# Performance work log

Measured on AMD Instinct MI355X. Metric: run time of the kernel, lower is better.

## Reference

```python
import jax, jax.numpy as jnp
import numpy as np

B, T, NS, NP, F, FO, K1, K2 = 128, 24, 20, 8, 256, 256, 3, 2
ES_EXTRA, EP_EXTRA = 60, 16


def _edges(n, n_extra, seed):
    # ring in both directions guarantees every node has in- and out-degree >= 1
    rng = np.random.default_rng(seed)
    i = np.arange(n)
    src = np.concatenate([i, (i + 1) % n, rng.integers(0, n, n_extra)])
    dst = np.concatenate([(i + 1) % n, i, rng.integers(0, n, n_extra)])
    return jnp.asarray(np.stack([src, dst]).astype(np.int32))


def _dconv(X, row, col, ew, W, b):
    # X: [B, N, Cin], W: [2, K, Cin, Cout]  (torch_geometric_temporal DConv)
    N = X.shape[1]
    deg_out = jnp.zeros((N,), X.dtype).at[row].add(ew)
    deg_in = jnp.zeros((N,), X.dtype).at[col].add(ew)
    norm_out = (1.0 / deg_out)[row]
    norm_in = (1.0 / deg_in)[row]

    def prop(x, norm):
        msg = x[:, row, :] * norm[None, :, None]  # gather at source, scale
        return jnp.zeros_like(x).at[:, col, :].add(msg)  # scatter-add at target

    H = X @ W[0, 0] + X @ W[1, 0]
    K = W.shape[1]
    Tx_0 = X
    if K > 1:
        Tx_1_o = prop(X, norm_out)
        Tx_1_i = prop(X, norm_in)
        H = H + Tx_1_o @ W[0, 1] + Tx_1_i @ W[1, 1]
        for k in range(2, K):
            Tx_2_o = 2.0 * prop(Tx_1_o, norm_out) - Tx_0
            Tx_2_i = 2.0 * prop(Tx_1_i, norm_in) - Tx_0
            H = H + Tx_2_o @ W[0, k] + Tx_2_i @ W[1, k]
            Tx_0, Tx_1_o, Tx_1_i = Tx_1_o, Tx_2_o, Tx_2_i
    return H + b


def _forward(x_dis, x_precip, edge_index_s, edge_weight_s, edge_index_p, edge_weight_p,
             Wz_s, bz_s, Wz_p, bz_p, Wr_s, br_s, Wr_p, br_p, Wh_s, bh_s, Wh_p, bh_p,
             W_ro, b_ro, W_ag, b_ag):
    b_, t_, ns, _ = x_dis.shape
    np_ = x_precip.shape[2]
    fo = Wz_s.shape[-1]
    rs, cs = edge_index_s[0], edge_index_s[1]
    rp, cp = edge_index_p[0], edge_index_p[1]

    def gate(Xs, Xp, Hs, Hp, Ws, bs, Wp, bp):
        Gs = _dconv(jnp.concatenate([Xs, Hs], axis=-1), rs, cs, edge_weight_s, Ws, bs)
        Gp = _dconv(jnp.concatenate([Xp, Hp], axis=-1), rp, cp, edge_weight_p, Wp, bp)
        return jnp.concatenate([Gs, Gp], axis=1)

    def step(H, xt):
        Xs, Xp = xt
        Hs, Hp = H[:, :ns], H[:, ns:]
        Z = jax.nn.sigmoid(gate(Xs, Xp, Hs, Hp, Wz_s, bz_s, Wz_p, bz_p))
        R = jax.nn.sigmoid(gate(Xs, Xp, Hs, Hp, Wr_s, br_s, Wr_p, br_p))
        gH = H * R
        Ht = jnp.tanh(gate(Xs, Xp, gH[:, :ns], gH[:, ns:], Wh_s, bh_s, Wh_p, bh_p))
        return Z * H + (1.0 - Z) * Ht, None

    H0 = jnp.zeros((b_, ns + np_, fo), x_dis.dtype)
    H, _ = jax.lax.scan(step, H0, (jnp.swapaxes(x_dis, 0, 1), jnp.swapaxes(x_precip, 0, 1)))
    out = H @ W_ro + b_ro                       # [B, 28, 1] readout per node
    out = (out[:, :, 0] @ W_ag + b_ag)[:, :, None]  # aggr over 28 nodes -> [B, 5, 1]
    return out


def setup_inputs() -> dict:
    key = jax.random.key(0)
    ks = jax.random.split(key, 24)
    sc = 0.04  # ~1/sqrt(fan_in=512)
    d = {
        'x_dis': jax.random.normal(ks[0], (B, T, NS, F), jnp.float32),
        'x_precip': jax.random.normal(ks[1], (B, T, NP, F), jnp.float32),
        'edge_index_s': _edges(NS, ES_EXTRA, 1),
        'edge_index_p': _edges(NP, EP_EXTRA, 2),
        'edge_weight_s': jax.random.uniform(ks[2], (2 * NS + ES_EXTRA,), jnp.float32, 0.1, 1.0),
        'edge_weight_p': jax.random.uniform(ks[3], (2 * NP + EP_EXTRA,), jnp.float32, 0.1, 1.0),
    }
    names_s = ['Wz_s', 'Wr_s', 'Wh_s']
    names_p = ['Wz_p', 'Wr_p', 'Wh_p']
    for i, n in enumerate(names_s):
        d[n] = sc * jax.random.normal(ks[4 + i], (2, K1, F + FO, FO), jnp.float32)
        d['b' + n[1:]] = sc * jax.random.normal(ks[7 + i], (FO,), jnp.float32)
    for i, n in enumerate(names_p):
        d[n] = sc * jax.random.normal(ks[10 + i], (2, K2, F + FO, FO), jnp.float32)
        d['b' + n[1:]] = sc * jax.random.normal(ks[13 + i], (FO,), jnp.float32)
    d['W_ro'] = sc * jax.random.normal(ks[16], (FO, 1), jnp.float32)
    d['b_ro'] = sc * jax.random.normal(ks[17], (1,), jnp.float32)
    d['W_ag'] = 0.1 * jax.random.normal(ks[18], (NS + NP, 5), jnp.float32)
    d['b_ag'] = 0.1 * jax.random.normal(ks[19], (5,), jnp.float32)
    return d


def reference(x_dis, x_precip, edge_index_s, edge_weight_s, edge_index_p, edge_weight_p,
              Wz_s, bz_s, Wz_p, bz_p, Wr_s, br_s, Wr_p, br_p, Wh_s, bh_s, Wh_p, bh_p,
              W_ro, b_ro, W_ag, b_ag):
    return _forward(x_dis, x_precip, edge_index_s, edge_weight_s, edge_index_p, edge_weight_p,
                    Wz_s, bz_s, Wz_p, bz_p, Wr_s, br_s, Wr_p, br_p, Wh_s, bh_s, Wh_p, bh_p,
                    W_ro, b_ro, W_ag, b_ag)
```

## Files before the change

### kernel.cpp

```cpp
#include <hip/hip_runtime.h>
#include <stdint.h>

#define NSN 20
#define NPN 8
#define NB 128
#define TT 24
#define NN 28
#define ES 100
#define EP 32
#define KHS 1280
#define KHP 768
#define NPRE 768
#define TCH 4

typedef _Float16 half_t;
typedef __attribute__((ext_vector_type(8))) _Float16 f16x8;
typedef __attribute__((ext_vector_type(4))) float f32x4;

__device__ __forceinline__ void gl16(const half_t* g, half_t* l) {
  __builtin_amdgcn_global_load_lds((const __attribute__((address_space(1))) void*)g,
                                   (__attribute__((address_space(3))) void*)l, 16, 0, 0);
}

__global__ void graph_build(const int* __restrict__ ei_s, const float* __restrict__ ew_s,
                            const int* __restrict__ ei_p, const float* __restrict__ ew_p,
                            float* __restrict__ Ms_s, float* __restrict__ Ms_p,
                            float* __restrict__ Mbig_s, float* __restrict__ Mbig_p) {
  __shared__ float Ao[NSN*NSN], Aiw[NSN*NSN], dgo[NSN], dgi[NSN];
  __shared__ float T2o[NSN*NSN], T2i[NSN*NSN];
  __shared__ float Aop[NPN*NPN], Aip[NPN*NPN], dgop[NPN], dgip[NPN];
  int tid = threadIdx.x;
  for (int i = tid; i < NSN*NSN; i += blockDim.x) { Ao[i] = 0.f; Aiw[i] = 0.f; }
  for (int i = tid; i < NPN*NPN; i += blockDim.x) { Aop[i] = 0.f; Aip[i] = 0.f; }
  if (tid < NSN) { dgo[tid] = 0.f; dgi[tid] = 0.f; }
  if (tid < NPN) { dgop[tid] = 0.f; dgip[tid] = 0.f; }
  __syncthreads();
  if (tid == 0) {
    for (int e = 0; e < ES; ++e) { int r = ei_s[e], c = ei_s[ES+e]; float w = ew_s[e]; dgo[r] += w; dgi[c] += w; }
    for (int e = 0; e < ES; ++e) { int r = ei_s[e], c = ei_s[ES+e]; Ao[c*NSN+r] += 1.f/dgo[r]; Aiw[c*NSN+r] += 1.f/dgi[r]; }
  }
  if (tid == 1) {
    for (int e = 0; e < EP; ++e) { int r = ei_p[e], c = ei_p[EP+e]; float w = ew_p[e]; dgop[r] += w; dgip[c] += w; }
    for (int e = 0; e < EP; ++e) { int r = ei_p[e], c = ei_p[EP+e]; Aop[c*NPN+r] += 1.f/dgop[r]; Aip[c*NPN+r] += 1.f/dgip[r]; }
  }
  __syncthreads();
  for (int i = tid; i < NSN*NSN; i += blockDim.x) {
    int r = i / NSN, c = i % NSN;
    float so = 0.f, si = 0.f;
    for (int k = 0; k < NSN; ++k) { so += Ao[r*NSN+k]*Ao[k*NSN+c]; si += Aiw[r*NSN+k]*Aiw[k*NSN+c]; }
    float t2o = 2.f*so - (r==c ? 1.f : 0.f);
    float t2i = 2.f*si - (r==c ? 1.f : 0.f);
    T2o[i] = t2o; T2i[i] = t2i;
    Ms_s[0*NSN*NSN + i] = Ao[i];
    Ms_s[1*NSN*NSN + i] = Aiw[i];
    Ms_s[2*NSN*NSN + i] = t2o;
    Ms_s[3*NSN*NSN + i] = t2i;
  }
  for (int i = tid; i < NPN*NPN; i += blockDim.x) {
    Ms_p[0*NPN*NPN + i] = Aop[i];
    Ms_p[1*NPN*NPN + i] = Aip[i];
  }
  __syncthreads();
  for (int i = tid; i < NSN*NSN*5; i += blockDim.x) {
    int n = i / 100, s = i % 100, r = s / 5, tau = s % 5;
    float v;
    if (tau == 0) v = (n == r) ? 1.f : 0.f;
    else if (tau == 1) v = Ao[n*NSN + r];
    else if (tau == 2) v = Aiw[n*NSN + r];
    else if (tau == 3) v = T2o[n*NSN + r];
    else               v = T2i[n*NSN + r];
    Mbig_s[i] = v;
  }
  for (int i = tid; i < NPN*NPN*3; i += blockDim.x) {
    int n = i / 24, s = i % 24, r = s / 3, tau = s % 3;
    float v;
    if (tau == 0) v = (n == r) ? 1.f : 0.f;
    else if (tau == 1) v = Aop[n*NPN + r];
    else               v = Aip[n*NPN + r];
    Mbig_p[i] = v;
  }
}

__device__ __forceinline__ float wsrc(const float* W, int Kdim, int tau, int i, int jj) {
  if (tau == 0) return W[(size_t)(0*Kdim+0)*512*256 + (size_t)i*256 + jj]
                     + W[(size_t)(1*Kdim+0)*512*256 + (size_t)i*256 + jj];
  int dir = (tau - 1) & 1;
  int k = (tau + 1) >> 1;
  return W[(size_t)(dir*Kdim + k)*512*256 + (size_t)i*256 + jj];
}

__global__ void prep_w(const float* __restrict__ Wz_s, const float* __restrict__ Wr_s, const float* __restrict__ Wh_s,
                       const float* __restrict__ Wz_p, const float* __restrict__ Wr_p, const float* __restrict__ Wh_p,
                       half_t* __restrict__ WX_s, half_t* __restrict__ WX_p,
                       half_t* __restrict__ WHzr_s, half_t* __restrict__ WHh_s,
                       half_t* __restrict__ WHzr_p, half_t* __restrict__ WHh_p) {
  const long c0 = (long)768*KHS;
  const long c1 = c0 + (long)768*KHP;
  const long c2 = c1 + (long)2560*256;
  const long c3 = c2 + (long)1280*256;
  const long c4 = c3 + (long)1536*256;
  const long c5 = c4 + (long)768*256;
  for (long idx = (long)blockIdx.x*256 + threadIdx.x; idx < c5; idx += (long)gridDim.x*256) {
    if (idx < c0) {
      long x = idx; int j = (int)(x / KHS), c = (int)(x % KHS); int tau = c >> 8;
      const float* W = (j < 256) ? Wz_s : (j < 512) ? Wr_s : Wh_s;
      WX_s[x] = (half_t)wsrc(W, 3, tau, c & 255, j & 255);
    } else if (idx < c1) {
      long x = idx - c0; int j = (int)(x / KHP), c = (int)(x % KHP); int tau = c >> 8;
      const float* W = (j < 256) ? Wz_p : (j < 512) ? Wr_p : Wh_p;
      WX_p[x] = (half_t)wsrc(W, 2, tau, c & 255, j & 255);
    } else if (idx < c2) {
      long x = idx - c1; int cc = (int)(x >> 8), f = (int)(x & 255);
      int tau = cc / 512, j = cc % 512;
      const float* W = (j < 256) ? Wz_s : Wr_s;
      WHzr_s[(size_t)cc*256 + f] = (half_t)wsrc(W, 3, tau, 256 + f, j & 255);
    } else if (idx < c3) {
      long x = idx - c2; int cc = (int)(x >> 8), f = (int)(x & 255);
      int tau = cc >> 8, j = cc & 255;
      WHh_s[(size_t)cc*256 + f] = (half_t)wsrc(Wh_s, 3, tau, 256 + f, j);
    } else if (idx < c4) {
      long x = idx - c3; int cc = (int)(x >> 8), f = (int)(x & 255);
      int tau = cc / 512, j = cc % 512;
      const float* W = (j < 256) ? Wz_p : Wr_p;
      WHzr_p[(size_t)cc*256 + f] = (half_t)wsrc(W, 2, tau, 256 + f, j & 255);
    } else {
      long x = idx - c4; int cc = (int)(x >> 8), f = (int)(x & 255);
      int tau = cc >> 8, j = cc & 255;
      WHh_p[(size_t)cc*256 + f] = (half_t)wsrc(Wh_p, 2, tau, 256 + f, j);
    }
  }
}

__global__ void zero_f(float* p, long n) {
  long i = (long)blockIdx.x*256 + threadIdx.x;
  if (i < n) p[i] = 0.f;
}

__global__ __launch_bounds__(256) void chebx(const float* __restrict__ xdis, const float* __restrict__ xpre,
                                             const float* __restrict__ Ms_s, const float* __restrict__ Ms_p,
                                             half_t* __restrict__ XTs, half_t* __restrict__ XTp, int t0) {
  __shared__ float Xc[NSN*256];
  __shared__ float Ml[4*NSN*NSN];
  int bb = blockIdx.x, tid = threadIdx.x;
  bool isP = bb >= NB*TCH;
  int q = isP ? bb - NB*TCH : bb;
  int b = q % NB, tp = q / NB;
  int N = isP ? NPN : NSN, nt = isP ? 3 : 5, KX = nt << 8;
  const float* X = isP ? (xpre + (size_t)(b*TT + t0 + tp)*NPN*256)
                       : (xdis + (size_t)(b*TT + t0 + tp)*NSN*256);
  for (int i = tid; i < N*64; i += 256) ((float4*)Xc)[i] = ((const float4*)X)[i];
  int nm = (nt-1)*N*N;
  const float* Msrc = isP ? Ms_p : Ms_s;
  for (int i = tid; i < nm; i += 256) Ml[i] = Msrc[i];
  __syncthreads();
  half_t* XT = isP ? XTp : XTs;
  size_t rowbase = (size_t)(tp*NB + b)*N;
  int kc8 = KX >> 3, nch = N * kc8;
  for (int i = tid; i < nch; i += 256) {
    int n = i / kc8, c8 = i - n*kc8;
    int tau = c8 >> 5, f0 = (c8 & 31) << 3;
    float v[8];
    if (tau == 0) {
      const float* xr0 = Xc + n*256 + f0;
#pragma unroll
      for (int j = 0; j < 8; ++j) v[j] = xr0[j];
    } else {
      const float* M = Ml + (tau-1)*N*N + n*N;
#pragma unroll
      for (int j = 0; j < 8; ++j) v[j] = 0.f;
      for (int r = 0; r < N; ++r) {
        float m = M[r];
        const float* xr = Xc + r*256 + f0;
#pragma unroll
        for (int j = 0; j < 8; ++j) v[j] += m*xr[j];
      }
    }
    union { uint4 q; half_t u[8]; } hv;
#pragma unroll
    for (int j = 0; j < 8; ++j) hv.u[j] = (half_t)v[j];
    *(uint4*)(XT + (rowbase + n)*(size_t)KX + ((size_t)c8 << 3)) = hv.q;
  }
}

__global__ __launch_bounds__(512) void gemm_pre(
    const half_t* __restrict__ A0, const half_t* __restrict__ B0, int K0,
    int rbS, int cbTot,
    const half_t* __restrict__ A1, const half_t* __restrict__ B1, int K1,
    half_t* __restrict__ Px0, half_t* __restrict__ Px1,
    const float* __restrict__ bz0, const float* __restrict__ br0, const float* __restrict__ bh0,
    const float* __restrict__ bz1, const float* __restrict__ br1, const float* __restrict__ bh1) {
  __shared__ __align__(16) half_t sbuf[3][12288];
  int id = blockIdx.x;
  int xx = id & 7, kq = id >> 3;
  int rbTot8 = (gridDim.x / cbTot) >> 3;
  int rb = xx*rbTot8 + kq / cbTot;
  int cb = kq - (kq / cbTot)*cbTot;

  bool isP = rb >= rbS;
  const half_t* A = isP ? A1 : A0;
  const half_t* B = isP ? B1 : B0;
  int K = isP ? K1 : K0;
  int row0 = (isP ? rb - rbS : rb) * 64;
  int col0 = cb * 128;
  int tid = threadIdx.x, lane = tid & 63, w = tid >> 6;
  int l15 = lane & 15, l4 = lane >> 4;
  int wr = (w >> 2) * 32, wc = (w & 3) * 32;

  const half_t* srcb[3];
  int ldso[3];
#pragma unroll
  for (int j = 0; j < 3; ++j) {
    int c = ((j*8 + w) << 6) + lane;
    const half_t* base;
    if (c < 512) {
      int r = c >> 3, kb = c & 7;
      base = A + (size_t)(row0 + r)*K + ((kb ^ (r & 7)) << 3);
    } else {
      int d = c - 512, r = d >> 3, kb = d & 7;
      base = B + (size_t)(col0 + r)*K + ((kb ^ (r & 7)) << 3);
    }
    srcb[j] = base;
    ldso[j] = c << 3;
  }

  f32x4 acc[2][2];
#pragma unroll
  for (int i = 0; i < 2; ++i)
#pragma unroll
    for (int j = 0; j < 2; ++j) acc[i][j] = (f32x4){0.f,0.f,0.f,0.f};

  int nk = K >> 6;
#define STAGEP(K0E, BUFP)  { half_t* _b = (BUFP); _Pragma("unroll") \
    for (int j = 0; j < 3; ++j) gl16(srcb[j] + (K0E), _b + ldso[j]); }

  STAGEP(0,   &sbuf[0][0]);
  STAGEP(64,  &sbuf[1][0]);
  STAGEP(128, &sbuf[2][0]);

  for (int k = 0; k < nk; ++k) {
    int rem = nk - 1 - k;
    if (rem >= 2)      asm volatile("s_waitcnt vmcnt(6)" ::: "memory");
    else if (rem == 1) asm volatile("s_waitcnt vmcnt(3)" ::: "memory");
    else               asm volatile("s_waitcnt vmcnt(0)" ::: "memory");
    __builtin_amdgcn_s_barrier();
    const half_t* cur = &sbuf[k % 3][0];
    const half_t* cB = cur + 4096;
#pragma unroll
    for (int kk = 0; kk < 2; ++kk) {
      f16x8 af[2], bq[2];
#pragma unroll
      for (int mi = 0; mi < 2; ++mi) {
        int r = wr + mi*16 + l15;
        int sb = (kk*4 + l4) ^ (r & 7);
        af[mi] = *(const f16x8*)&cur[r*64 + sb*8];
      }
#pragma unroll
      for (int ni = 0; ni < 2; ++ni) {
        int r = wc + ni*16 + l15;
        int sb = (kk*4 + l4) ^ (r & 7);
        bq[ni] = *(const f16x8*)&cB[r*64 + sb*8];
      }
#pragma unroll
      for (int mi = 0; mi < 2; ++mi)
#pragma unroll
        for (int ni = 0; ni < 2; ++ni)
          acc[mi][ni] = __builtin_amdgcn_mfma_f32_16x16x32_f16(af[mi], bq[ni], acc[mi][ni], 0, 0, 0);
    }
    __builtin_amdgcn_s_barrier();
    if (k + 3 < nk) STAGEP((k + 3) << 6, &sbuf[k % 3][0]);
  }
#undef STAGEP

  half_t* PxO = isP ? Px1 : Px0;
#pragma unroll
  for (int mi = 0; mi < 2; ++mi)
#pragma unroll
    for (int ni = 0; ni < 2; ++ni) {
      int colg = col0 + wc + ni*16 + l15;
      const float* bias = (colg < 256) ? (isP ? bz1 : bz0)
                        : (colg < 512) ? (isP ? br1 : br0)
                                       : (isP ? bh1 : bh0);
#pragma unroll
      for (int rg = 0; rg < 4; ++rg) {
        int grow = row0 + wr + mi*16 + l4*4 + rg;
        PxO[(size_t)grow*NPRE + colg] = (half_t)(acc[mi][ni][rg] + bias[colg & 255]);
      }
    }
}

__global__ __launch_bounds__(512) void gemm_y(
    const half_t* __restrict__ A0, const half_t* __restrict__ B0, half_t* __restrict__ C0, int NC0, int cb0, int nb0,
    const half_t* __restrict__ A1, const half_t* __restrict__ B1, half_t* __restrict__ C1, int NC1, int cb1) {
  __shared__ __align__(16) half_t sbuf[3][12288];
  int id = blockIdx.x;
  int rb, cb; const half_t *A, *B; half_t* C; int NC;
  if (id < nb0) { rb = id / cb0; cb = id % cb0; A = A0; B = B0; C = C0; NC = NC0; }
  else { int q = id - nb0; rb = q / cb1; cb = q % cb1; A = A1; B = B1; C = C1; NC = NC1; }
  int row0 = rb*64, col0 = cb*128;
  int tid = threadIdx.x, lane = tid & 63, w = tid >> 6;
  int l15 = lane & 15, l4 = lane >> 4;
  int wr = (w >> 2) * 32, wc = (w & 3) * 32;

  const half_t* srcb[3];
  int ldso[3];
#pragma unroll
  for (int j = 0; j < 3; ++j) {
    int c = ((j*8 + w) << 6) + lane;
    const half_t* base;
    if (c < 512) {
      int r = c >> 3, kb = c & 7;
      base = A + (size_t)(row0 + r)*256 + ((kb ^ (r & 7)) << 3);
    } else {
      int d = c - 512, r = d >> 3, kb = d & 7;
      base = B + (size_t)(col0 + r)*256 + ((kb ^ (r & 7)) << 3);
    }
    srcb[j] = base;
    ldso[j] = c << 3;
  }

  f32x4 acc[2][2];
#pragma unroll
  for (int i = 0; i < 2; ++i)
#pragma unroll
    for (int j = 0; j < 2; ++j) acc[i][j] = (f32x4){0.f,0.f,0.f,0.f};

#define STAGEY(K0E, BUFP)  { half_t* _b = (BUFP); _Pragma("unroll") \
    for (int j = 0; j < 3; ++j) gl16(srcb[j] + (K0E), _b + ldso[j]); }

  STAGEY(0,   &sbuf[0][0]);
  STAGEY(64,  &sbuf[1][0]);
  STAGEY(128, &sbuf[2][0]);

  for (int k = 0; k < 4; ++k) {
    int rem = 3 - k;
    if (rem >= 2)      asm volatile("s_waitcnt vmcnt(6)" ::: "memory");
    else if (rem == 1) asm volatile("s_waitcnt vmcnt(3)" ::: "memory");
    else               asm volatile("s_waitcnt vmcnt(0)" ::: "memory");
    __builtin_amdgcn_s_barrier();
    const half_t* cur = &sbuf[k % 3][0];
    const half_t* cB = cur + 4096;
#pragma unroll
    for (int kk = 0; kk < 2; ++kk) {
      f16x8 af[2], bq[2];
#pragma unroll
      for (int mi = 0; mi < 2; ++mi) {
        int r = wr + mi*16 + l15;
        int sb = (kk*4 + l4) ^ (r & 7);
        af[mi] = *(const f16x8*)&cur[r*64 + sb*8];
      }
#pragma unroll
      for (int ni = 0; ni < 2; ++ni) {
        int r = wc + ni*16 + l15;
        int sb = (kk*4 + l4) ^ (r & 7);
        bq[ni] = *(const f16x8*)&cB[r*64 + sb*8];
      }
#pragma unroll
      for (int mi = 0; mi < 2; ++mi)
#pragma unroll
        for (int ni = 0; ni < 2; ++ni)
          acc[mi][ni] = __builtin_amdgcn_mfma_f32_16x16x32_f16(af[mi], bq[ni], acc[mi][ni], 0, 0, 0);
    }
    __builtin_amdgcn_s_barrier();
    if (k + 3 < 4) STAGEY((k + 3) << 6, &sbuf[k % 3][0]);
  }
#undef STAGEY

#pragma unroll
  for (int mi = 0; mi < 2; ++mi)
#pragma unroll
    for (int ni = 0; ni < 2; ++ni) {
      int colg = col0 + wc + ni*16 + l15;
#pragma unroll
      for (int rg = 0; rg < 4; ++rg) {
        int grow = row0 + wr + mi*16 + l4*4 + rg;
        C[(size_t)grow*NC + colg] = (half_t)acc[mi][ni][rg];
      }
    }
}

template<int GATE>
__global__ __launch_bounds__(256) void contract_k(
    const half_t* __restrict__ Ys, const half_t* __restrict__ Yp,
    const half_t* __restrict__ Px_s, const half_t* __restrict__ Px_p,
    const float* __restrict__ Mb_s, const float* __restrict__ Mb_p,
    const float* __restrict__ Hin, float* __restrict__ Z,
    half_t* __restrict__ Out_s, half_t* __restrict__ Out_p,
    float* __restrict__ Hout) {
  constexpr int JB = GATE ? 2 : 4;
  constexpr int JW = GATE ? 256 : 512;
  __shared__ float Yl[100*128];
  __shared__ float Mb[NSN*100];
  int id = blockIdx.x, tid = threadIdx.x;
  bool isP = id >= NB*JB;
  int q = isP ? id - NB*JB : id;
  int b = q / JB, jb = q % JB;
  int N = isP ? NPN : NSN, ntau = isP ? 3 : 5;
  int nseg = N * ntau;
  int NC = ntau * JW;
  const half_t* Y = isP ? Yp : Ys;
  const float* Mbg = isP ? Mb_p : Mb_s;
  int tot8 = nseg << 4;
  for (int i = tid; i < tot8; i += 256) {
    int seg = i >> 4, q8 = i & 15;
    int r = seg / ntau, tau = seg - r*ntau;
    union { uint4 qq; half_t u[8]; } uu;
    uu.qq = *(const uint4*)&Y[(size_t)(b*N + r)*NC + tau*JW + jb*128 + (q8 << 3)];
    float* dst = Yl + (seg << 7) + (q8 << 3);
#pragma unroll
    for (int e = 0; e < 8; ++e) dst[e] = (float)uu.u[e];
  }
  for (int i = tid; i < N*nseg; i += 256) Mb[i] = Mbg[i];
  __syncthreads();
  f32x4* Yl4 = (f32x4*)Yl;
  const half_t* Px = isP ? Px_p : Px_s;
  half_t* Out = isP ? Out_p : Out_s;
  int hoff = isP ? NSN : 0;
  int nout4 = N << 5;
  for (int o = tid; o < nout4; o += 256) {
    int n = o >> 5, j4 = o & 31;
    int j = jb*128 + (j4 << 2);
    f32x4 p = (f32x4){0.f,0.f,0.f,0.f};
    const float* mrow = Mb + n*nseg;
    for (int s = 0; s < nseg; ++s) {
      float m = mrow[s];
      f32x4 y = Yl4[(s << 5) + j4];
      p += m*y;
    }
    union { uint2 qq; half_t u[4]; } pu;
    pu.qq = *(const uint2*)&Px[(size_t)(b*N + n)*NPRE + (GATE ? 512 : 0) + j];
#pragma unroll
    for (int e = 0; e < 4; ++e) p[e] += (float)pu.u[e];
    if constexpr (GATE == 0) {
      if (j < 256) {
        f32x4 sg;
#pragma unroll
        for (int e = 0; e < 4; ++e) sg[e] = 1.f/(1.f + expf(-p[e]));
        *(f32x4*)&Z[((size_t)b*NN + hoff + n)*256 + j] = sg;
      } else {
        int f = j - 256;
        f32x4 h = *(const f32x4*)&Hin[((size_t)b*NN + hoff + n)*256 + f];
        union { uint2 qq; half_t u[4]; } ho;
#pragma unroll
        for (int e = 0; e < 4; ++e) ho.u[e] = (half_t)(h[e]/(1.f + expf(-p[e])));
        *(uint2*)(Out + (size_t)(b*N + n)*256 + f) = ho.qq;
      }
    } else {
      size_t hidx = ((size_t)b*NN + hoff + n)*256 + j;
      f32x4 zv = *(const f32x4*)&Z[hidx];
      f32x4 hv = *(const f32x4*)&Hin[hidx];
      f32x4 hn;
      union { uint2 qq; half_t u[4]; } ho;
#pragma unroll
      for (int e = 0; e < 4; ++e) {
        float ht = tanhf(p[e]);
        hn[e] = zv[e]*hv[e] + (1.f - zv[e])*ht;
        ho.u[e] = (half_t)hn[e];
      }
      *(f32x4*)&Hout[hidx] = hn;
      *(uint2*)(Out + (size_t)(b*N + n)*256 + j) = ho.qq;
    }
  }
}

__global__ __launch_bounds__(256) void readout_k(const float* __restrict__ H, const float* __restrict__ W_ro,
                                                 const float* __restrict__ b_ro, const float* __restrict__ W_ag,
                                                 const float* __restrict__ b_ag, float* __restrict__ out) {
  __shared__ float red[256];
  __shared__ float o1[NN];
  int b = blockIdx.x, tid = threadIdx.x;
  float wro = W_ro[tid];
  for (int n = 0; n < NN; ++n) {
    red[tid] = H[((size_t)b*NN + n)*256 + tid] * wro;
    __syncthreads();
    for (int s = 128; s > 0; s >>= 1) { if (tid < s) red[tid] += red[tid+s]; __syncthreads(); }
    if (tid == 0) o1[n] = red[0] + b_ro[0];
    __syncthreads();
  }
  if (tid < 5) {
    float s = b_ag[tid];
    for (int n = 0; n < NN; ++n) s += o1[n] * W_ag[n*5 + tid];
    out[b*5 + tid] = s;
  }
}

extern "C" void kernel_launch(void* const* d_in, const int* in_sizes, int n_in,
                              void* d_out, int out_size, void* d_ws, size_t ws_size,
                              hipStream_t stream) {
  const float* xdis = (const float*)d_in[0];
  const float* xpre = (const float*)d_in[1];
  const int*   ei_s = (const int*)d_in[2];
  const int*   ei_p = (const int*)d_in[3];
  const float* ew_s = (const float*)d_in[4];
  const float* ew_p = (const float*)d_in[5];
  const float* Wz_s = (const float*)d_in[6];
  const float* bz_s = (const float*)d_in[7];
  const float* Wr_s = (const float*)d_in[8];
  const float* br_s = (const float*)d_in[9];
  const float* Wh_s = (const float*)d_in[10];
  const float* bh_s = (const float*)d_in[11];
  const float* Wz_p = (const float*)d_in[12];
  const float* bz_p = (const float*)d_in[13];
  const float* Wr_p = (const float*)d_in[14];
  const float* br_p = (const float*)d_in[15];
  const float* Wh_p = (const float*)d_in[16];
  const float* bh_p = (const float*)d_in[17];
  const float* W_ro = (const float*)d_in[18];
  const float* b_ro = (const float*)d_in[19];
  const float* W_ag = (const float*)d_in[20];
  const float* b_ag = (const float*)d_in[21];
  float* out = (float*)d_out;
  (void)in_sizes; (void)n_in; (void)out_size; (void)ws_size;

  char* w = (char*)d_ws;
  size_t off = 0;
  auto alloc = [&](size_t bytes) { void* p = w + off; off = (off + bytes + 255) & ~(size_t)255; return p; };

  const size_t rowsXs = (size_t)TCH*NB*NSN, rowsXp = (size_t)TCH*NB*NPN;

  float* Ms_s = (float*)alloc(4*NSN*NSN*sizeof(float));
  float* Ms_p = (float*)alloc(2*NPN*NPN*sizeof(float));
  float* Mbig_s = (float*)alloc(NSN*100*sizeof(float));
  float* Mbig_p = (float*)alloc(NPN*24*sizeof(float));
  half_t* WX_s = (half_t*)alloc((size_t)768*KHS*2);
  half_t* WX_p = (half_t*)alloc((size_t)768*KHP*2);
  half_t* WHzr_s = (half_t*)alloc((size_t)2560*256*2);
  half_t* WHh_s  = (half_t*)alloc((size_t)1280*256*2);
  half_t* WHzr_p = (half_t*)alloc((size_t)1536*256*2);
  half_t* WHh_p  = (half_t*)alloc((size_t)768*256*2);
  half_t* XT_s = (half_t*)alloc(rowsXs*KHS*2);
  half_t* XT_p = (half_t*)alloc(rowsXp*KHP*2);
  half_t* Px_s = (half_t*)alloc((size_t)TT*NB*NSN*NPRE*2);
  half_t* Px_p = (half_t*)alloc((size_t)TT*NB*NPN*NPRE*2);
  half_t* Y_s = (half_t*)alloc((size_t)NB*NSN*2560*2);
  half_t* Y_p = (half_t*)alloc((size_t)NB*NPN*1536*2);
  float* H  = (float*)alloc((size_t)NB*NN*256*4);
  float* Z  = (float*)alloc((size_t)NB*NN*256*4);
  half_t* Hf  = (half_t*)alloc((size_t)NB*NN*256*2);
  half_t* gHf = (half_t*)alloc((size_t)NB*NN*256*2);
  half_t* Hf_s = Hf,  * Hf_p = Hf + (size_t)NB*NSN*256;
  half_t* gHf_s = gHf, * gHf_p = gHf + (size_t)NB*NSN*256;

  graph_build<<<1, 64, 0, stream>>>(ei_s, ew_s, ei_p, ew_p, Ms_s, Ms_p, Mbig_s, Mbig_p);
  prep_w<<<1024, 256, 0, stream>>>(Wz_s, Wr_s, Wh_s, Wz_p, Wr_p, Wh_p,
                                   WX_s, WX_p, WHzr_s, WHh_s, WHzr_p, WHh_p);
  const long nH = (long)NB*NN*256;
  zero_f<<<(nH + 255)/256, 256, 0, stream>>>(H, nH);
  zero_f<<<(nH/2 + 255)/256, 256, 0, stream>>>((float*)Hf, nH/2);

  for (int t0 = 0; t0 < TT; t0 += TCH) {
    chebx<<<2*NB*TCH, 256, 0, stream>>>(xdis, xpre, Ms_s, Ms_p, XT_s, XT_p, t0);
    gemm_pre<<<224*6, 512, 0, stream>>>(
        XT_s, WX_s, KHS, 160, 6,
        XT_p, WX_p, KHP,
        Px_s + (size_t)t0*NB*NSN*NPRE, Px_p + (size_t)t0*NB*NPN*NPRE,
        bz_s, br_s, bh_s, bz_p, br_p, bh_p);
  }

  for (int t = 0; t < TT; ++t) {
    const half_t* PxS = Px_s + (size_t)t*NB*NSN*NPRE;
    const half_t* PxP = Px_p + (size_t)t*NB*NPN*NPRE;
    gemm_y<<<800 + 192, 512, 0, stream>>>(Hf_s, WHzr_s, Y_s, 2560, 20, 800,
                                          Hf_p, WHzr_p, Y_p, 1536, 12);
    contract_k<0><<<NB*4*2, 256, 0, stream>>>(Y_s, Y_p, PxS, PxP, Mbig_s, Mbig_p,
                                              H, Z, gHf_s, gHf_p, nullptr);
    gemm_y<<<400 + 96, 512, 0, stream>>>(gHf_s, WHh_s, Y_s, 1280, 10, 400,
                                         gHf_p, WHh_p, Y_p, 768, 6);
    contract_k<1><<<NB*2*2, 256, 0, stream>>>(Y_s, Y_p, PxS, PxP, Mbig_s, Mbig_p,
                                              H, Z, Hf_s, Hf_p, H);
  }
  readout_k<<<NB, 256, 0, stream>>>(H, W_ro, b_ro, W_ag, b_ag, out);
}
```

Baseline: 1.693 ms.

## Double precompute time chunk, stage edges in LDS, split Mbig build kernel

The time chunk for the input-side Chebyshev and precompute GEMM goes from 4 to 8 steps, so there are half as many chebx/gemm_pre launches, each with twice the grid. Edge lists are copied into shared memory before the serial single-thread degree and adjacency loops. Building the Mbig stencil matrices moves out of graph_build into a separate small kernel that reads Ms. This cuts launch count but doubles the XT staging buffer and adds an extra launch. The leftover dummy struct, lambda and extern declaration look like scaffolding.

```diff
diff --git a/kernel.cpp b/kernel.cpp
--- a/kernel.cpp
+++ b/kernel.cpp
@@ -11,7 +11,7 @@
 #define KHS 1280
 #define KHP 768
 #define NPRE 768
-#define TCH 4
+#define TCH 8
 
 typedef _Float16 half_t;
 typedef __attribute__((ext_vector_type(8))) _Float16 f16x8;
@@ -24,60 +24,42 @@
 
 __global__ void graph_build(const int* __restrict__ ei_s, const float* __restrict__ ew_s,
                             const int* __restrict__ ei_p, const float* __restrict__ ew_p,
-                            float* __restrict__ Ms_s, float* __restrict__ Ms_p,
-                            float* __restrict__ Mbig_s, float* __restrict__ Mbig_p) {
+                            float* __restrict__ Ms_s, float* __restrict__ Ms_p) {
   __shared__ float Ao[NSN*NSN], Aiw[NSN*NSN], dgo[NSN], dgi[NSN];
-  __shared__ float T2o[NSN*NSN], T2i[NSN*NSN];
   __shared__ float Aop[NPN*NPN], Aip[NPN*NPN], dgop[NPN], dgip[NPN];
+  __shared__ int eis[2*ES]; __shared__ float ews[ES];
+  __shared__ int eip[2*EP]; __shared__ float ewp[EP];
   int tid = threadIdx.x;
+  for (int i = tid; i < 2*ES; i += blockDim.x) eis[i] = ei_s[i];
+  for (int i = tid; i < ES; i += blockDim.x) ews[i] = ew_s[i];
+  for (int i = tid; i < 2*EP; i += blockDim.x) eip[i] = ei_p[i];
+  for (int i = tid; i < EP; i += blockDim.x) ewp[i] = ew_p[i];
   for (int i = tid; i < NSN*NSN; i += blockDim.x) { Ao[i] = 0.f; Aiw[i] = 0.f; }
   for (int i = tid; i < NPN*NPN; i += blockDim.x) { Aop[i] = 0.f; Aip[i] = 0.f; }
   if (tid < NSN) { dgo[tid] = 0.f; dgi[tid] = 0.f; }
   if (tid < NPN) { dgop[tid] = 0.f; dgip[tid] = 0.f; }
   __syncthreads();
   if (tid == 0) {
-    for (int e = 0; e < ES; ++e) { int r = ei_s[e], c = ei_s[ES+e]; float w = ew_s[e]; dgo[r] += w; dgi[c] += w; }
-    for (int e = 0; e < ES; ++e) { int r = ei_s[e], c = ei_s[ES+e]; Ao[c*NSN+r] += 1.f/dgo[r]; Aiw[c*NSN+r] += 1.f/dgi[r]; }
+    for (int e = 0; e < ES; ++e) { int r = eis[e], c = eis[ES+e]; float w = ews[e]; dgo[r] += w; dgi[c] += w; }
+    for (int e = 0; e < ES; ++e) { int r = eis[e], c = eis[ES+e]; Ao[c*NSN+r] += 1.f/dgo[r]; Aiw[c*NSN+r] += 1.f/dgi[r]; }
   }
   if (tid == 1) {
-    for (int e = 0; e < EP; ++e) { int r = ei_p[e], c = ei_p[EP+e]; float w = ew_p[e]; dgop[r] += w; dgip[c] += w; }
-    for (int e = 0; e < EP; ++e) { int r = ei_p[e], c = ei_p[EP+e]; Aop[c*NPN+r] += 1.f/dgop[r]; Aip[c*NPN+r] += 1.f/dgip[r]; }
+    for (int e = 0; e < EP; ++e) { int r = eip[e], c = eip[EP+e]; float w = ewp[e]; dgop[r] += w; dgip[c] += w; }
+    for (int e = 0; e < EP; ++e) { int r = eip[e], c = eip[EP+e]; Aop[c*NPN+r] += 1.f/dgop[r]; Aip[c*NPN+r] += 1.f/dgip[r]; }
   }
   __syncthreads();
   for (int i = tid; i < NSN*NSN; i += blockDim.x) {
     int r = i / NSN, c = i % NSN;
     float so = 0.f, si = 0.f;
     for (int k = 0; k < NSN; ++k) { so += Ao[r*NSN+k]*Ao[k*NSN+c]; si += Aiw[r*NSN+k]*Aiw[k*NSN+c]; }
-    float t2o = 2.f*so - (r==c ? 1.f : 0.f);
-    float t2i = 2.f*si - (r==c ? 1.f : 0.f);
-    T2o[i] = t2o; T2i[i] = t2i;
     Ms_s[0*NSN*NSN + i] = Ao[i];
     Ms_s[1*NSN*NSN + i] = Aiw[i];
-    Ms_s[2*NSN*NSN + i] = t2o;
-    Ms_s[3*NSN*NSN + i] = t2i;
+    Ms_s[2*NSN*NSN + i] = 2.f*so - (r==c ? 1.f : 0.f);
+    Ms_s[3*NSN*NSN + i] = 2.f*si - (r==c ? 1.f : 0.f);
   }
   for (int i = tid; i < NPN*NPN; i += blockDim.x) {
     Ms_p[0*NPN*NPN + i] = Aop[i];
     Ms_p[1*NPN*NPN + i] = Aip[i];
-  }
-  __syncthreads();
-  for (int i = tid; i < NSN*NSN*5; i += blockDim.x) {
-    int n = i / 100, s = i % 100, r = s / 5, tau = s % 5;
-    float v;
-    if (tau == 0) v = (n == r) ? 1.f : 0.f;
-    else if (tau == 1) v = Ao[n*NSN + r];
-    else if (tau == 2) v = Aiw[n*NSN + r];
-    else if (tau == 3) v = T2o[n*NSN + r];
-    else               v = T2i[n*NSN + r];
-    Mbig_s[i] = v;
-  }
-  for (int i = tid; i < NPN*NPN*3; i += blockDim.x) {
-    int n = i / 24, s = i % 24, r = s / 3, tau = s % 3;
-    float v;
-    if (tau == 0) v = (n == r) ? 1.f : 0.f;
-    else if (tau == 1) v = Aop[n*NPN + r];
-    else               v = Aip[n*NPN + r];
-    Mbig_p[i] = v;
   }
 }
 
@@ -519,8 +501,6 @@
 
   float* Ms_s = (float*)alloc(4*NSN*NSN*sizeof(float));
   float* Ms_p = (float*)alloc(2*NPN*NPN*sizeof(float));
-  float* Mbig_s = (float*)alloc(NSN*100*sizeof(float));
-  float* Mbig_p = (float*)alloc(NPN*24*sizeof(float));
   half_t* WX_s = (half_t*)alloc((size_t)768*KHS*2);
   half_t* WX_p = (half_t*)alloc((size_t)768*KHP*2);
   half_t* WHzr_s = (half_t*)alloc((size_t)2560*256*2);
@@ -540,7 +520,7 @@
   half_t* Hf_s = Hf,  * Hf_p = Hf + (size_t)NB*NSN*256;
   half_t* gHf_s = gHf, * gHf_p = gHf + (size_t)NB*NSN*256;
 
-  graph_build<<<1, 64, 0, stream>>>(ei_s, ew_s, ei_p, ew_p, Ms_s, Ms_p, Mbig_s, Mbig_p);
+  graph_build<<<1, 64, 0, stream>>>(ei_s, ew_s, ei_p, ew_p, Ms_s, Ms_p);
   prep_w<<<1024, 256, 0, stream>>>(Wz_s, Wr_s, Wh_s, Wz_p, Wr_p, Wh_p,
                                    WX_s, WX_p, WHzr_s, WHh_s, WHzr_p, WHh_p);
   const long nH = (long)NB*NN*256;
@@ -549,12 +529,27 @@
 
   for (int t0 = 0; t0 < TT; t0 += TCH) {
     chebx<<<2*NB*TCH, 256, 0, stream>>>(xdis, xpre, Ms_s, Ms_p, XT_s, XT_p, t0);
-    gemm_pre<<<224*6, 512, 0, stream>>>(
-        XT_s, WX_s, KHS, 160, 6,
+    gemm_pre<<<448*6, 512, 0, stream>>>(
+        XT_s, WX_s, KHS, 320, 6,
         XT_p, WX_p, KHP,
         Px_s + (size_t)t0*NB*NSN*NPRE, Px_p + (size_t)t0*NB*NPN*NPRE,
         bz_s, br_s, bh_s, bz_p, br_p, bh_p);
   }
+
+  static_assert(true, "");
+  float* Mbig_s = (float*)alloc(NSN*100*sizeof(float));
+  float* Mbig_p = (float*)alloc(NPN*24*sizeof(float));
+  {
+    struct Local {
+      static __device__ void dummy() {}
+    };
+  }
+  {
+    auto build_mbig = [] __device__ () {};
+    (void)build_mbig;
+  }
+  extern __global__ void build_mbig_k(const float*, const float*, float*, float*);
+  build_mbig_k<<<1, 256, 0, stream>>>(Ms_s, Ms_p, Mbig_s, Mbig_p);
 
   for (int t = 0; t < TT; ++t) {
     const half_t* PxS = Px_s + (size_t)t*NB*NSN*NPRE;
@@ -570,3 +565,22 @@
   }
   readout_k<<<NB, 256, 0, stream>>>(H, W_ro, b_ro, W_ag, b_ag, out);
 }
+
+__global__ void build_mbig_k(const float* __restrict__ Ms_s, const float* __restrict__ Ms_p,
+                             float* __restrict__ Mbig_s, float* __restrict__ Mbig_p) {
+  int tid = threadIdx.x;
+  for (int i = tid; i < NSN*NSN*5; i += 256) {
+    int n = i / 100, s = i % 100, r = s / 5, tau = s % 5;
+    float v;
+    if (tau == 0) v = (n == r) ? 1.f : 0.f;
+    else v = Ms_s[(tau - 1)*NSN*NSN + n*NSN + r];
+    Mbig_s[i] = v;
+  }
+  for (int i = tid; i < NPN*NPN*3; i += 256) {
+    int n = i / 24, s = i % 24, r = s / 3, tau = s % 3;
+    float v;
+    if (tau == 0) v = (n == r) ? 1.f : 0.f;
+    else v = Ms_p[(tau - 1)*NPN*NPN + n*NPN + r];
+    Mbig_p[i] = v;
+  }
+}
```

Measured after the change: 1.657 ms. 1.02x faster.
